# Kernel optimization log

Measured on AMD Instinct MI355X. Metric: run time of the kernel, lower is better.

## Reference

```python
import jax, jax.numpy as jnp
import numpy as np

B, T, D, H = 8, 2048, 1024, 64

def setup_inputs() -> dict:
    key = jax.random.key(0)
    kx, kq, kk, kv = jax.random.split(key, 4)
    x = jax.random.normal(kx, (B, T, D), dtype=jnp.float32)
    # Linear(embd_size, head_size, bias=False) weights, stored as [D, H] for x @ W
    Wq = jax.random.normal(kq, (D, H), dtype=jnp.float32) * (D ** -0.5)
    Wk = jax.random.normal(kk, (D, H), dtype=jnp.float32) * (D ** -0.5)
    Wv = jax.random.normal(kv, (D, H), dtype=jnp.float32) * (D ** -0.5)
    return {"x": x, "Wq": Wq, "Wk": Wk, "Wv": Wv}

def reference(x, Wq, Wk, Wv):
    Tcur = x.shape[1]
    q = x @ Wq  # [B, T, H]
    k = x @ Wk
    v = x @ Wv
    scores = jnp.einsum('bth,bsh->bts', q, k)
    # NOTE: faithful to source quirk: scores are MULTIPLIED by sqrt(T)
    scores = scores * (Tcur ** 0.5)
    causal = jnp.tril(jnp.ones((Tcur, Tcur), dtype=bool))
    scores = jnp.where(causal, scores, -jnp.inf)
    attn = jax.nn.softmax(scores, axis=2)  # dropout p=0.0 -> identity
    return jnp.einsum('bts,bsh->bth', attn, v)
```

## Files before the change

### kernel.cpp

```cpp
#include <hip/hip_runtime.h>
#include <hip/hip_bf16.h>

#define BB 8
#define TT 2048
#define DD 1024
#define HH 64
#define NROWS (BB*TT)
#define SCALE 45.25483399593904f
#define SPLIT 4

typedef __attribute__((ext_vector_type(8))) short short8;
typedef __attribute__((ext_vector_type(4))) float f32x4;

__device__ inline ushort bf16rne(float f) {
    unsigned u = __float_as_uint(f);
    return (ushort)((u + 0x7fffu + ((u >> 16) & 1u)) >> 16);
}
__device__ inline void bfsplit(float f, ushort& hi, ushort& lo) {
    hi = bf16rne(f);
    float fh = __uint_as_float(((unsigned)hi) << 16);
    lo = bf16rne(f - fh);
}
__device__ inline void split_pack8(const float* v, int4& h4, int4& l4) {
    ushort h[8], l[8];
    #pragma unroll
    for (int j = 0; j < 8; ++j) bfsplit(v[j], h[j], l[j]);
    h4 = make_int4((int)(h[0] | ((unsigned)h[1] << 16)), (int)(h[2] | ((unsigned)h[3] << 16)),
                   (int)(h[4] | ((unsigned)h[5] << 16)), (int)(h[6] | ((unsigned)h[7] << 16)));
    l4 = make_int4((int)(l[0] | ((unsigned)l[1] << 16)), (int)(l[2] | ((unsigned)l[3] << 16)),
                   (int)(l[4] | ((unsigned)l[5] << 16)), (int)(l[6] | ((unsigned)l[7] << 16)));
}

__device__ inline void gload_lds16(const void* g, void* l) {
    __builtin_amdgcn_global_load_lds(
        (const __attribute__((address_space(1))) unsigned int*)(uintptr_t)(g),
        (__attribute__((address_space(3))) unsigned int*)(uintptr_t)(l),
        16, 0, 0);
}

__global__ __launch_bounds__(256) void wprep_kernel(
        const float* __restrict__ Wq, const float* __restrict__ Wk,
        const float* __restrict__ Wv,
        ushort* __restrict__ WpHi, ushort* __restrict__ WpLo) {
    __shared__ float ws[64 * 65];
    const int m = blockIdx.x >> 4;
    const int c = blockIdx.x & 15;
    const float* W = (m == 0) ? Wq : (m == 1) ? Wk : Wv;
    const int tid = threadIdx.x;

    #pragma unroll
    for (int p = 0; p < 4; ++p) {
        int i = tid + p * 256;
        int r = i >> 4, q4 = i & 15;
        float4 v = *(const float4*)(W + (size_t)(c * 64 + r) * 64 + q4 * 4);
        ws[r * 65 + q4 * 4 + 0] = v.x;
        ws[r * 65 + q4 * 4 + 1] = v.y;
        ws[r * 65 + q4 * 4 + 2] = v.z;
        ws[r * 65 + q4 * 4 + 3] = v.w;
    }
    __syncthreads();

    #pragma unroll
    for (int p = 0; p < 2; ++p) {
        int gi = tid + p * 256;
        int nn = gi >> 3, g8 = gi & 7;
        int o  = g8 ^ (nn & 7);
        float v[8];
        #pragma unroll
        for (int j = 0; j < 8; ++j) v[j] = ws[(o * 8 + j) * 65 + nn];
        int4 h4, l4; split_pack8(v, h4, l4);
        size_t base = (size_t)c * 12288 + (size_t)(m * 64 + nn) * 64 + g8 * 8;
        *(int4*)(WpHi + base) = h4;
        *(int4*)(WpLo + base) = l4;
    }
}

__global__ __launch_bounds__(512) void qkv_kernel(
        const float* __restrict__ x,
        const ushort* __restrict__ WpHi, const ushort* __restrict__ WpLo,
        float* __restrict__ Qo, ushort* __restrict__ KhiP,
        ushort* __restrict__ KloP, ushort* __restrict__ VtP) {
    __shared__ ushort Ahi[64 * 64], Alo[64 * 64];
    __shared__ ushort Bhi[2][192 * 64], Blo[2][192 * 64];
    const int tid  = threadIdx.x;
    const int lane = tid & 63;
    const int w    = tid >> 6;
    const int wm   = w >> 2;
    const int wn   = w & 3;
    const int n15  = lane & 15;
    const int g    = lane >> 4;
    const int csw  = n15 & 7;
    const int row0 = blockIdx.x * 64;

    f32x4 acc[2][3];
    #pragma unroll
    for (int ms = 0; ms < 2; ++ms)
        #pragma unroll
        for (int nt = 0; nt < 3; ++nt) acc[ms][nt] = (f32x4)0.f;

    const int ar = tid >> 3, aoc = tid & 7;
    const float* xrow = x + (size_t)(row0 + ar) * 1024 + aoc * 8;
    const int adi = ar * 64 + ((aoc ^ (ar & 7)) << 3);

    const ushort* wsh = WpHi + (size_t)lane * 8;
    const ushort* wsl = WpLo + (size_t)lane * 8;

    #pragma unroll
    for (int p = 0; p < 3; ++p) {
        int j = w * 3 + p;
        gload_lds16(wsh + j * 512, &Bhi[0][j * 512]);
        gload_lds16(wsl + j * 512, &Blo[0][j * 512]);
    }
    float xv[8];
    *(float4*)(xv)     = *(const float4*)(xrow);
    *(float4*)(xv + 4) = *(const float4*)(xrow + 4);

    int cur = 0;
    for (int c = 0; c < 16; ++c) {
        const int c1 = (c + 1 < 16) ? c + 1 : 15;
        {
            const ushort* sh = wsh + (size_t)c1 * 12288;
            const ushort* sl = wsl + (size_t)c1 * 12288;
            #pragma unroll
            for (int p = 0; p < 3; ++p) {
                int j = w * 3 + p;
                gload_lds16(sh + j * 512, &Bhi[cur ^ 1][j * 512]);
                gload_lds16(sl + j * 512, &Blo[cur ^ 1][j * 512]);
            }
        }
        asm volatile("s_waitcnt vmcnt(6)" ::: "memory");
        __builtin_amdgcn_sched_barrier(0);
        {
            int4 h4, l4; split_pack8(xv, h4, l4);
            *(int4*)&Ahi[adi] = h4;
            *(int4*)&Alo[adi] = l4;
        }
        {
            const float* src = xrow + (size_t)c1 * 64;
            *(float4*)(xv)     = *(const float4*)(src);
            *(float4*)(xv + 4) = *(const float4*)(src + 4);
        }
        asm volatile("s_waitcnt lgkmcnt(0)" ::: "memory");
        __builtin_amdgcn_s_barrier();
        __builtin_amdgcn_sched_barrier(0);

        #pragma unroll
        for (int kh = 0; kh < 2; ++kh) {
            short8 afh[2], afl[2], bfh[3], bfl[3];
            #pragma unroll
            for (int ms = 0; ms < 2; ++ms) {
                int ao = (wm * 32 + ms * 16 + n15) * 64 + (((4 * kh + g) ^ csw) << 3);
                afh[ms] = *(const short8*)&Ahi[ao];
                afl[ms] = *(const short8*)&Alo[ao];
            }
            #pragma unroll
            for (int nt = 0; nt < 3; ++nt) {
                int bo = (wn * 48 + nt * 16 + n15) * 64 + (((4 * kh + g) ^ csw) << 3);
                bfh[nt] = *(const short8*)&Bhi[cur][bo];
                bfl[nt] = *(const short8*)&Blo[cur][bo];
            }
            #pragma unroll
            for (int nt = 0; nt < 3; ++nt)
                #pragma unroll
                for (int ms = 0; ms < 2; ++ms) {
                    acc[ms][nt] = __builtin_amdgcn_mfma_f32_16x16x32_bf16(
                        afh[ms], bfh[nt], acc[ms][nt], 0, 0, 0);
                    acc[ms][nt] = __builtin_amdgcn_mfma_f32_16x16x32_bf16(
                        afl[ms], bfh[nt], acc[ms][nt], 0, 0, 0);
                    acc[ms][nt] = __builtin_amdgcn_mfma_f32_16x16x32_bf16(
                        afh[ms], bfl[nt], acc[ms][nt], 0, 0, 0);
                }
        }
        __builtin_amdgcn_s_barrier();
        cur ^= 1;
    }

    const int b  = row0 >> 11;
    const int t0 = row0 & 2047;
    #pragma unroll
    for (int nt = 0; nt < 3; ++nt) {
        const int col = wn * 48 + nt * 16 + n15;
        const int mat = col >> 6;
        const int h   = col & 63;
        #pragma unroll
        for (int ms = 0; ms < 2; ++ms) {
            const int mb = row0 + wm * 32 + ms * 16 + 4 * g;
            if (mat == 0) {
                #pragma unroll
                for (int r = 0; r < 4; ++r)
                    Qo[(size_t)(mb + r) * 64 + h] = acc[ms][nt][r];
            } else if (mat == 1) {
                #pragma unroll
                for (int r = 0; r < 4; ++r) {
                    ushort hi, lo; bfsplit(acc[ms][nt][r], hi, lo);
                    KhiP[(size_t)(mb + r) * 64 + h] = hi;
                    KloP[(size_t)(mb + r) * 64 + h] = lo;
                }
            } else {
                ushort pk[4];
                #pragma unroll
                for (int r = 0; r < 4; ++r) pk[r] = bf16rne(acc[ms][nt][r]);
                const int tloc = t0 + wm * 32 + ms * 16 + 4 * g;
                *(uint2*)&VtP[((size_t)(b * 64 + h)) * 2048 + tloc] =
                    make_uint2(pk[0] | ((unsigned)pk[1] << 16),
                               pk[2] | ((unsigned)pk[3] << 16));
            }
        }
    }
}

__global__ __launch_bounds__(128) void attn_kernel(
        const float* __restrict__ Q, const ushort* __restrict__ Khi,
        const ushort* __restrict__ Klo, const ushort* __restrict__ Vt,
        float* __restrict__ Pacc, float* __restrict__ Pm,
        float* __restrict__ Pl) {
    __shared__ ushort KhiL[64 * 64];
    __shared__ ushort KloL[64 * 64];
    __shared__ ushort VtL[64 * 64];
    const int tid  = threadIdx.x;
    const int lane = tid & 63;
    const int w    = tid >> 6;
    const int n    = lane & 15;
    const int g    = lane >> 4;
    const int b    = blockIdx.y;
    const int xx   = blockIdx.x;
    const int qt   = 63 - (xx >> 2);
    const int sp   = xx & 3;
    const int q0   = qt * 32;
    const int qmin = q0 + w * 16;
    const int qrow = qmin + n;
    const int csw  = n & 7;
    const int ntiles = (q0 >> 6) + 1;
    const int it0  = (ntiles * sp) >> 2;
    const int it1  = (ntiles * (sp + 1)) >> 2;

    short8 qhi0, qhi1, qlo0, qlo1;
    {
        const float* qp = Q + ((size_t)b * TT + qrow) * HH + 8 * g;
        float v0[8], v1[8];
        *(float4*)(v0)     = *(const float4*)(qp);
        *(float4*)(v0 + 4) = *(const float4*)(qp + 4);
        *(float4*)(v1)     = *(const float4*)(qp + 32);
        *(float4*)(v1 + 4) = *(const float4*)(qp + 36);
        #pragma unroll
        for (int j = 0; j < 8; ++j) {
            ushort hi, lo;
            bfsplit(v0[j], hi, lo); qhi0[j] = (short)hi; qlo0[j] = (short)lo;
            bfsplit(v1[j], hi, lo); qhi1[j] = (short)hi; qlo1[j] = (short)lo;
        }
    }

    f32x4 accO[4];
    #pragma unroll
    for (int t = 0; t < 4; ++t) accO[t] = (f32x4)0.f;
    float m = -1e30f, l = 0.f;

    const ushort* gkh = Khi + (size_t)b * TT * HH;
    const ushort* gkl = Klo + (size_t)b * TT * HH;
    const ushort* gvt = Vt + (size_t)b * 64 * TT;

    const int crow = lane >> 3;
    const int coct = lane & 7;

    for (int it = it0; it < it1; ++it) {
        const int kb = it * 64;
        __syncthreads();
        #pragma unroll
        for (int p = 0; p < 4; ++p) {
            const int cc  = w * 4 + p;
            const int row = (cc << 3) + crow;
            const int soc = coct ^ (row & 7);
            gload_lds16(gkh + (size_t)(kb + row) * HH + (soc << 3), &KhiL[cc << 9]);
            gload_lds16(gkl + (size_t)(kb + row) * HH + (soc << 3), &KloL[cc << 9]);
            gload_lds16(gvt + (size_t)row * TT + kb + (soc << 3),   &VtL[cc << 9]);
        }
        __syncthreads();

        f32x4 s4[4];
        #pragma unroll
        for (int s = 0; s < 4; ++s) {
            const int keyl = 16 * s + n;
            const ushort* kbase = &KhiL[keyl << 6];
            const ushort* lbase = &KloL[keyl << 6];
            short8 kh0 = *(const short8*)(kbase + ((g ^ csw) << 3));
            short8 kh1 = *(const short8*)(kbase + (((4 + g) ^ csw) << 3));
            short8 kl0 = *(const short8*)(lbase + ((g ^ csw) << 3));
            short8 kl1 = *(const short8*)(lbase + (((4 + g) ^ csw) << 3));
            f32x4 a = (f32x4)0.f;
            a = __builtin_amdgcn_mfma_f32_16x16x32_bf16(kh0, qhi0, a, 0, 0, 0);
            a = __builtin_amdgcn_mfma_f32_16x16x32_bf16(kh1, qhi1, a, 0, 0, 0);
            a = __builtin_amdgcn_mfma_f32_16x16x32_bf16(kl0, qhi0, a, 0, 0, 0);
            a = __builtin_amdgcn_mfma_f32_16x16x32_bf16(kl1, qhi1, a, 0, 0, 0);
            a = __builtin_amdgcn_mfma_f32_16x16x32_bf16(kh0, qlo0, a, 0, 0, 0);
            a = __builtin_amdgcn_mfma_f32_16x16x32_bf16(kh1, qlo1, a, 0, 0, 0);
            s4[s] = a;
        }

        float sm[16];
        if (kb + 63 > qmin) {
            #pragma unroll
            for (int s = 0; s < 4; ++s)
                #pragma unroll
                for (int r = 0; r < 4; ++r) {
                    int keyg = kb + 16 * s + 4 * g + r;
                    sm[s * 4 + r] = (keyg <= qrow) ? s4[s][r] * SCALE : -1e30f;
                }
        } else {
            #pragma unroll
            for (int s = 0; s < 4; ++s)
                #pragma unroll
                for (int r = 0; r < 4; ++r) sm[s * 4 + r] = s4[s][r] * SCALE;
        }
        float pm = sm[0];
        #pragma unroll
        for (int i = 1; i < 16; ++i) pm = fmaxf(pm, sm[i]);
        pm = fmaxf(pm, __shfl_xor(pm, 16));
        pm = fmaxf(pm, __shfl_xor(pm, 32));
        float mn = fmaxf(m, pm);
        float es = __expf(m - mn);
        float p[16], ps = 0.f;
        #pragma unroll
        for (int i = 0; i < 16; ++i) { p[i] = __expf(sm[i] - mn); ps += p[i]; }
        ps += __shfl_xor(ps, 16);
        ps += __shfl_xor(ps, 32);
        l = l * es + ps;
        m = mn;
        #pragma unroll
        for (int t = 0; t < 4; ++t)
            #pragma unroll
            for (int r = 0; r < 4; ++r) accO[t][r] *= es;

        short8 pf0, pf1;
        #pragma unroll
        for (int j = 0; j < 4; ++j) {
            pf0[j]     = (short)bf16rne(p[0 * 4 + j]);
            pf0[j + 4] = (short)bf16rne(p[1 * 4 + j]);
            pf1[j]     = (short)bf16rne(p[2 * 4 + j]);
            pf1[j + 4] = (short)bf16rne(p[3 * 4 + j]);
        }

        #pragma unroll
        for (int t = 0; t < 4; ++t) {
            const int h = 16 * t + n;
            const ushort* vb = &VtL[h << 6];
            union { int2 d[2]; short8 v; } u0, u1;
            u0.d[0] = *(const int2*)(vb + ((4 * g) ^ (csw << 3)));
            u0.d[1] = *(const int2*)(vb + ((16 + 4 * g) ^ (csw << 3)));
            u1.d[0] = *(const int2*)(vb + ((32 + 4 * g) ^ (csw << 3)));
            u1.d[1] = *(const int2*)(vb + ((48 + 4 * g) ^ (csw << 3)));
            accO[t] = __builtin_amdgcn_mfma_f32_16x16x32_bf16(u0.v, pf0, accO[t], 0, 0, 0);
            accO[t] = __builtin_amdgcn_mfma_f32_16x16x32_bf16(u1.v, pf1, accO[t], 0, 0, 0);
        }
    }

    const size_t brow = (size_t)b * TT + qrow;
    float* pa = Pacc + ((size_t)sp * NROWS + brow) * 64 + 4 * g;
    #pragma unroll
    for (int t = 0; t < 4; ++t)
        *(f32x4*)(pa + 16 * t) = accO[t];
    if (g == 0) {
        Pm[(size_t)sp * NROWS + brow] = m;
        Pl[(size_t)sp * NROWS + brow] = l;
    }
}

__global__ __launch_bounds__(256) void combine_kernel(
        const float* __restrict__ Pacc, const float* __restrict__ Pm,
        const float* __restrict__ Pl, float* __restrict__ out) {
    const int u    = blockIdx.x * 256 + threadIdx.x;
    const int row  = u >> 2;
    const int quad = u & 3;

    float ms[SPLIT], ls[SPLIT], M = -1e30f;
    #pragma unroll
    for (int s = 0; s < SPLIT; ++s) {
        ms[s] = Pm[(size_t)s * NROWS + row];
        ls[s] = Pl[(size_t)s * NROWS + row];
        M = fmaxf(M, ms[s]);
    }
    float wgt[SPLIT], den = 0.f;
    #pragma unroll
    for (int s = 0; s < SPLIT; ++s) {
        wgt[s] = __expf(ms[s] - M);
        den += wgt[s] * ls[s];
    }
    const float inv = 1.0f / den;

    float4 o[4];
    #pragma unroll
    for (int i = 0; i < 4; ++i) o[i] = make_float4(0.f, 0.f, 0.f, 0.f);
    #pragma unroll
    for (int s = 0; s < SPLIT; ++s) {
        const float4* a = (const float4*)(Pacc + ((size_t)s * NROWS + row) * 64 + quad * 16);
        #pragma unroll
        for (int i = 0; i < 4; ++i) {
            float4 v = a[i];
            o[i].x += wgt[s] * v.x; o[i].y += wgt[s] * v.y;
            o[i].z += wgt[s] * v.z; o[i].w += wgt[s] * v.w;
        }
    }
    float4* op = (float4*)(out + (size_t)row * 64 + quad * 16);
    #pragma unroll
    for (int i = 0; i < 4; ++i)
        op[i] = make_float4(o[i].x * inv, o[i].y * inv, o[i].z * inv, o[i].w * inv);
}

extern "C" void kernel_launch(void* const* d_in, const int* in_sizes, int n_in,
                              void* d_out, int out_size, void* d_ws, size_t ws_size,
                              hipStream_t stream) {
    const float* x  = (const float*)d_in[0];
    const float* Wq = (const float*)d_in[1];
    const float* Wk = (const float*)d_in[2];
    const float* Wv = (const float*)d_in[3];
    float* outp = (float*)d_out;

    float*  Qw   = (float*)d_ws;
    ushort* KhiP = (ushort*)(Qw + (size_t)NROWS * HH);
    ushort* KloP = KhiP + (size_t)NROWS * HH;
    ushort* VtP  = KloP + (size_t)NROWS * HH;
    ushort* WpHi = VtP + (size_t)NROWS * HH;
    ushort* WpLo = WpHi + (size_t)3 * 64 * 1024;
    float*  Pacc = (float*)(WpLo + (size_t)3 * 64 * 1024);
    float*  Pm   = Pacc + (size_t)SPLIT * NROWS * HH;
    float*  Pl   = Pm + (size_t)SPLIT * NROWS;

    wprep_kernel<<<48, 256, 0, stream>>>(Wq, Wk, Wv, WpHi, WpLo);
    qkv_kernel<<<NROWS / 64, 512, 0, stream>>>(x, WpHi, WpLo, Qw, KhiP, KloP, VtP);
    attn_kernel<<<dim3(64 * SPLIT, BB), 128, 0, stream>>>(Qw, KhiP, KloP, VtP,
                                                          Pacc, Pm, Pl);
    combine_kernel<<<NROWS * 4 / 256, 256, 0, stream>>>(Pacc, Pm, Pl, outp);
}
```

Before: 71.20 us.

## Drop V low-part weight split and store split-K partials as bf16

The QKV projection now keeps only the bf16 high part of Wv and packs the Q/K low parts into a single 320-column weight buffer, which cuts a third of the correction MFMAs for V and shrinks the LDS and global weight traffic. The attention kernel's split partial accumulators are written as bf16 instead of fp32, and the combine kernel reads them at half the bytes. Together these lower memory traffic and MFMA count, at the cost of precision in V and in the un-normalized partial outputs.

New measurement: 70.32 us. No clear change (-1.2%).

```diff
diff --git a/kernel.cpp b/kernel.cpp
--- a/kernel.cpp
+++ b/kernel.cpp
@@ -8,6 +8,7 @@
 #define NROWS (BB*TT)
 #define SCALE 45.25483399593904f
 #define SPLIT 4
+#define BCOLS 320
 
 typedef __attribute__((ext_vector_type(8))) short short8;
 typedef __attribute__((ext_vector_type(4))) float f32x4;
@@ -30,6 +31,9 @@
     l4 = make_int4((int)(l[0] | ((unsigned)l[1] << 16)), (int)(l[2] | ((unsigned)l[3] << 16)),
                    (int)(l[4] | ((unsigned)l[5] << 16)), (int)(l[6] | ((unsigned)l[7] << 16)));
 }
+__device__ inline float bf2f(unsigned u16) {
+    return __uint_as_float(u16 << 16);
+}
 
 __device__ inline void gload_lds16(const void* g, void* l) {
     __builtin_amdgcn_global_load_lds(
@@ -40,8 +44,7 @@
 
 __global__ __launch_bounds__(256) void wprep_kernel(
         const float* __restrict__ Wq, const float* __restrict__ Wk,
-        const float* __restrict__ Wv,
-        ushort* __restrict__ WpHi, ushort* __restrict__ WpLo) {
+        const float* __restrict__ Wv, ushort* __restrict__ Wp) {
     __shared__ float ws[64 * 65];
     const int m = blockIdx.x >> 4;
     const int c = blockIdx.x & 15;
@@ -69,19 +72,19 @@
         #pragma unroll
         for (int j = 0; j < 8; ++j) v[j] = ws[(o * 8 + j) * 65 + nn];
         int4 h4, l4; split_pack8(v, h4, l4);
-        size_t base = (size_t)c * 12288 + (size_t)(m * 64 + nn) * 64 + g8 * 8;
-        *(int4*)(WpHi + base) = h4;
-        *(int4*)(WpLo + base) = l4;
+        const size_t cb = (size_t)c * (BCOLS * 64);
+        *(int4*)(Wp + cb + (size_t)(m * 64 + nn) * 64 + g8 * 8) = h4;
+        if (m < 2)
+            *(int4*)(Wp + cb + (size_t)(192 + m * 64 + nn) * 64 + g8 * 8) = l4;
     }
 }
 
 __global__ __launch_bounds__(512) void qkv_kernel(
-        const float* __restrict__ x,
-        const ushort* __restrict__ WpHi, const ushort* __restrict__ WpLo,
+        const float* __restrict__ x, const ushort* __restrict__ Wp,
         float* __restrict__ Qo, ushort* __restrict__ KhiP,
         ushort* __restrict__ KloP, ushort* __restrict__ VtP) {
     __shared__ ushort Ahi[64 * 64], Alo[64 * 64];
-    __shared__ ushort Bhi[2][192 * 64], Blo[2][192 * 64];
+    __shared__ ushort Bp[2][BCOLS * 64];
     const int tid  = threadIdx.x;
     const int lane = tid & 63;
     const int w    = tid >> 6;
@@ -102,14 +105,12 @@
     const float* xrow = x + (size_t)(row0 + ar) * 1024 + aoc * 8;
     const int adi = ar * 64 + ((aoc ^ (ar & 7)) << 3);
 
-    const ushort* wsh = WpHi + (size_t)lane * 8;
-    const ushort* wsl = WpLo + (size_t)lane * 8;
-
-    #pragma unroll
-    for (int p = 0; p < 3; ++p) {
-        int j = w * 3 + p;
-        gload_lds16(wsh + j * 512, &Bhi[0][j * 512]);
-        gload_lds16(wsl + j * 512, &Blo[0][j * 512]);
+    const ushort* wsp = Wp + (size_t)lane * 8;
+
+    #pragma unroll
+    for (int p = 0; p < 5; ++p) {
+        int j = w * 5 + p;
+        gload_lds16(wsp + j * 512, &Bp[0][j * 512]);
     }
     float xv[8];
     *(float4*)(xv)     = *(const float4*)(xrow);
@@ -119,16 +120,14 @@
     for (int c = 0; c < 16; ++c) {
         const int c1 = (c + 1 < 16) ? c + 1 : 15;
         {
-            const ushort* sh = wsh + (size_t)c1 * 12288;
-            const ushort* sl = wsl + (size_t)c1 * 12288;
-            #pragma unroll
-            for (int p = 0; p < 3; ++p) {
-                int j = w * 3 + p;
-                gload_lds16(sh + j * 512, &Bhi[cur ^ 1][j * 512]);
-                gload_lds16(sl + j * 512, &Blo[cur ^ 1][j * 512]);
+            const ushort* s = wsp + (size_t)c1 * (BCOLS * 64);
+            #pragma unroll
+            for (int p = 0; p < 5; ++p) {
+                int j = w * 5 + p;
+                gload_lds16(s + j * 512, &Bp[cur ^ 1][j * 512]);
             }
         }
-        asm volatile("s_waitcnt vmcnt(6)" ::: "memory");
+        asm volatile("s_waitcnt vmcnt(5)" ::: "memory");
         __builtin_amdgcn_sched_barrier(0);
         {
             int4 h4, l4; split_pack8(xv, h4, l4);
@@ -146,30 +145,33 @@
 
         #pragma unroll
         for (int kh = 0; kh < 2; ++kh) {
-            short8 afh[2], afl[2], bfh[3], bfl[3];
+            const int ko = ((4 * kh + g) ^ csw) << 3;
+            short8 afh[2], afl[2];
             #pragma unroll
             for (int ms = 0; ms < 2; ++ms) {
-                int ao = (wm * 32 + ms * 16 + n15) * 64 + (((4 * kh + g) ^ csw) << 3);
+                int ao = (wm * 32 + ms * 16 + n15) * 64 + ko;
                 afh[ms] = *(const short8*)&Ahi[ao];
                 afl[ms] = *(const short8*)&Alo[ao];
             }
             #pragma unroll
             for (int nt = 0; nt < 3; ++nt) {
-                int bo = (wn * 48 + nt * 16 + n15) * 64 + (((4 * kh + g) ^ csw) << 3);
-                bfh[nt] = *(const short8*)&Bhi[cur][bo];
-                bfl[nt] = *(const short8*)&Blo[cur][bo];
-            }
-            #pragma unroll
-            for (int nt = 0; nt < 3; ++nt)
+                const int colb = wn * 48 + nt * 16;
+                short8 bfh = *(const short8*)&Bp[cur][(colb + n15) * 64 + ko];
                 #pragma unroll
                 for (int ms = 0; ms < 2; ++ms) {
                     acc[ms][nt] = __builtin_amdgcn_mfma_f32_16x16x32_bf16(
-                        afh[ms], bfh[nt], acc[ms][nt], 0, 0, 0);
+                        afh[ms], bfh, acc[ms][nt], 0, 0, 0);
                     acc[ms][nt] = __builtin_amdgcn_mfma_f32_16x16x32_bf16(
-                        afl[ms], bfh[nt], acc[ms][nt], 0, 0, 0);
-                    acc[ms][nt] = __builtin_amdgcn_mfma_f32_16x16x32_bf16(
-                        afh[ms], bfl[nt], acc[ms][nt], 0, 0, 0);
+                        afl[ms], bfh, acc[ms][nt], 0, 0, 0);
                 }
+                if (colb < 128) {
+                    short8 bfl = *(const short8*)&Bp[cur][(192 + colb + n15) * 64 + ko];
+                    #pragma unroll
+                    for (int ms = 0; ms < 2; ++ms)
+                        acc[ms][nt] = __builtin_amdgcn_mfma_f32_16x16x32_bf16(
+                            afh[ms], bfl, acc[ms][nt], 0, 0, 0);
+                }
+            }
         }
         __builtin_amdgcn_s_barrier();
         cur ^= 1;
@@ -212,7 +214,7 @@
 __global__ __launch_bounds__(128) void attn_kernel(
         const float* __restrict__ Q, const ushort* __restrict__ Khi,
         const ushort* __restrict__ Klo, const ushort* __restrict__ Vt,
-        float* __restrict__ Pacc, float* __restrict__ Pm,
+        ushort* __restrict__ PaccH, float* __restrict__ Pm,
         float* __restrict__ Pl) {
     __shared__ ushort KhiL[64 * 64];
     __shared__ ushort KloL[64 * 64];
@@ -354,10 +356,14 @@
     }
 
     const size_t brow = (size_t)b * TT + qrow;
-    float* pa = Pacc + ((size_t)sp * NROWS + brow) * 64 + 4 * g;
-    #pragma unroll
-    for (int t = 0; t < 4; ++t)
-        *(f32x4*)(pa + 16 * t) = accO[t];
+    ushort* pa = PaccH + ((size_t)sp * NROWS + brow) * 64 + 4 * g;
+    #pragma unroll
+    for (int t = 0; t < 4; ++t) {
+        ushort e0 = bf16rne(accO[t][0]), e1 = bf16rne(accO[t][1]);
+        ushort e2 = bf16rne(accO[t][2]), e3 = bf16rne(accO[t][3]);
+        *(uint2*)(pa + 16 * t) = make_uint2(e0 | ((unsigned)e1 << 16),
+                                            e2 | ((unsigned)e3 << 16));
+    }
     if (g == 0) {
         Pm[(size_t)sp * NROWS + brow] = m;
         Pl[(size_t)sp * NROWS + brow] = l;
@@ -365,7 +371,7 @@
 }
 
 __global__ __launch_bounds__(256) void combine_kernel(
-        const float* __restrict__ Pacc, const float* __restrict__ Pm,
+        const ushort* __restrict__ PaccH, const float* __restrict__ Pm,
         const float* __restrict__ Pl, float* __restrict__ out) {
     const int u    = blockIdx.x * 256 + threadIdx.x;
     const int row  = u >> 2;
@@ -391,12 +397,14 @@
     for (int i = 0; i < 4; ++i) o[i] = make_float4(0.f, 0.f, 0.f, 0.f);
     #pragma unroll
     for (int s = 0; s < SPLIT; ++s) {
-        const float4* a = (const float4*)(Pacc + ((size_t)s * NROWS + row) * 64 + quad * 16);
+        const ushort* a = PaccH + ((size_t)s * NROWS + row) * 64 + quad * 16;
         #pragma unroll
         for (int i = 0; i < 4; ++i) {
-            float4 v = a[i];
-            o[i].x += wgt[s] * v.x; o[i].y += wgt[s] * v.y;
-            o[i].z += wgt[s] * v.z; o[i].w += wgt[s] * v.w;
+            uint2 uv = *(const uint2*)(a + i * 4);
+            o[i].x += wgt[s] * bf2f(uv.x & 0xffffu);
+            o[i].y += wgt[s] * bf2f(uv.x >> 16);
+            o[i].z += wgt[s] * bf2f(uv.y & 0xffffu);
+            o[i].w += wgt[s] * bf2f(uv.y >> 16);
         }
     }
     float4* op = (float4*)(out + (size_t)row * 64 + quad * 16);
@@ -414,19 +422,18 @@
     const float* Wv = (const float*)d_in[3];
     float* outp = (float*)d_out;
 
-    float*  Qw   = (float*)d_ws;
-    ushort* KhiP = (ushort*)(Qw + (size_t)NROWS * HH);
-    ushort* KloP = KhiP + (size_t)NROWS * HH;
-    ushort* VtP  = KloP + (size_t)NROWS * HH;
-    ushort* WpHi = VtP + (size_t)NROWS * HH;
-    ushort* WpLo = WpHi + (size_t)3 * 64 * 1024;
-    float*  Pacc = (float*)(WpLo + (size_t)3 * 64 * 1024);
-    float*  Pm   = Pacc + (size_t)SPLIT * NROWS * HH;
-    float*  Pl   = Pm + (size_t)SPLIT * NROWS;
-
-    wprep_kernel<<<48, 256, 0, stream>>>(Wq, Wk, Wv, WpHi, WpLo);
-    qkv_kernel<<<NROWS / 64, 512, 0, stream>>>(x, WpHi, WpLo, Qw, KhiP, KloP, VtP);
+    float*  Qw    = (float*)d_ws;
+    ushort* KhiP  = (ushort*)(Qw + (size_t)NROWS * HH);
+    ushort* KloP  = KhiP + (size_t)NROWS * HH;
+    ushort* VtP   = KloP + (size_t)NROWS * HH;
+    ushort* Wp    = VtP + (size_t)NROWS * HH;
+    ushort* PaccH = Wp + (size_t)16 * BCOLS * 64;
+    float*  Pm    = (float*)(PaccH + (size_t)SPLIT * NROWS * HH);
+    float*  Pl    = Pm + (size_t)SPLIT * NROWS;
+
+    wprep_kernel<<<48, 256, 0, stream>>>(Wq, Wk, Wv, Wp);
+    qkv_kernel<<<NROWS / 64, 512, 0, stream>>>(x, Wp, Qw, KhiP, KloP, VtP);
     attn_kernel<<<dim3(64 * SPLIT, BB), 128, 0, stream>>>(Qw, KhiP, KloP, VtP,
-                                                          Pacc, Pm, Pl);
-    combine_kernel<<<NROWS * 4 / 256, 256, 0, stream>>>(Pacc, Pm, Pl, outp);
-}
+                                                          PaccH, Pm, Pl);
+    combine_kernel<<<NROWS * 4 / 256, 256, 0, stream>>>(PaccH, Pm, Pl, outp);
+}
```
